# Optimization experiments

Hardware: AMD Instinct MI355X
Metric: run time of the kernel (lower is better)

## Reference

```python
import jax, jax.numpy as jnp
import numpy as np
import math

HEADS = 16
ROPE_BASE = 10000.0


def _alibi_slopes(n):
    # power-of-2 branch of ALiBiBias._get_slopes (n=16 is a power of 2)
    start = 2.0 ** (-(2.0 ** (-(math.log2(n) - 3))))
    return np.array([start * (start ** i) for i in range(n)], dtype=np.float32)


def _rope_cos_sin(T, head_dim):
    # RotaryPositionalEmbedding: inv_freq over even indices, emb = cat(freqs, freqs)
    inv_freq = 1.0 / (ROPE_BASE ** (jnp.arange(0, head_dim, 2, dtype=jnp.float32) / head_dim))
    t = jnp.arange(T, dtype=jnp.float32)
    f = t[:, None] * inv_freq[None, :]            # (T, head_dim//2)
    emb = jnp.concatenate([f, f], axis=-1)        # (T, head_dim)
    # apply_rotary_pos_emb takes cos/sin of emb then strides [0::2]
    cos = jnp.cos(emb)[:, 0::2]                   # (T, head_dim//2)
    sin = jnp.sin(emb)[:, 0::2]
    return cos, sin


def _apply_rope(x, cos, sin):
    # x: (B,H,T,hd); cos/sin: (T, hd//2)
    x1 = x[..., 0::2]
    x2 = x[..., 1::2]
    r1 = x1 * cos - x2 * sin
    r2 = x2 * cos + x1 * sin
    # interleave back: out[...,0::2]=r1, out[...,1::2]=r2
    return jnp.stack([r1, r2], axis=-1).reshape(x.shape)


def setup_inputs() -> dict:
    key = jax.random.key(0)
    k1, k2, k3, k4 = jax.random.split(key, 4)
    B, T, C = 2, 2048, 1024
    x = jax.random.normal(k1, (B, T, C), dtype=jnp.float32)
    W_qkv = jax.random.normal(k2, (C, 3 * C), dtype=jnp.float32) * 0.02
    W_out = jax.random.normal(k3, (C, C), dtype=jnp.float32) * 0.02
    b_out = jax.random.normal(k4, (C,), dtype=jnp.float32) * 0.02
    return {"x": x, "W_qkv": W_qkv, "W_out": W_out, "b_out": b_out}


def reference(x, W_qkv, W_out, b_out):
    B, T, C = x.shape
    H = HEADS
    hd = C // H

    qkv = (x @ W_qkv).reshape(B, T, 3, H, hd)
    qkv = jnp.transpose(qkv, (2, 0, 3, 1, 4))     # (3, B, H, T, hd)
    q, k, v = qkv[0], qkv[1], qkv[2]

    cos, sin = _rope_cos_sin(T, hd)
    q = _apply_rope(q, cos, sin)
    k = _apply_rope(k, cos, sin)

    scores = jnp.einsum('bhqd,bhkd->bhqk', q, k) / jnp.sqrt(jnp.float32(hd))

    # ALiBi bias: -slope_h * |i - j|
    slopes = jnp.asarray(_alibi_slopes(H))        # (H,)
    pos = jnp.arange(T, dtype=jnp.float32)
    dist = jnp.abs(pos[None, :] - pos[:, None])   # (T, T)
    scores = scores - slopes[None, :, None, None] * dist[None, None, :, :]

    attn = jax.nn.softmax(scores, axis=-1)
    out = jnp.einsum('bhqk,bhkd->bhqd', attn, v)  # (B,H,T,hd)
    out = jnp.transpose(out, (0, 2, 1, 3)).reshape(B, T, C)
    out = out @ W_out + b_out
    return out, attn
```

## Files before the change

### kernel.cpp

```cpp
#include <hip/hip_runtime.h>
#include <hip/hip_bf16.h>

typedef __bf16 bf16_t;
typedef __bf16 bf16x8 __attribute__((ext_vector_type(8)));
typedef __bf16 bf16x4 __attribute__((ext_vector_type(4)));
typedef float floatx4 __attribute__((ext_vector_type(4)));

#define NB 2
#define NT 2048
#define NC 1024
#define NH 16
#define HD 64
#define BT (NB*NT)

#define GLL16(g, l) __builtin_amdgcn_global_load_lds( \
    (const __attribute__((address_space(1))) void*)(g), \
    (__attribute__((address_space(3))) void*)(l), 16, 0, 0)

__global__ void k_cvt_x(const float* __restrict__ x, bf16_t* __restrict__ xb, int n){
  int i = (blockIdx.x*blockDim.x + threadIdx.x)*4;
  if (i >= n) return;
  float4 v = *(const float4*)(x+i);
  bf16_t o[4] = {(bf16_t)v.x,(bf16_t)v.y,(bf16_t)v.z,(bf16_t)v.w};
  *(uint2*)(xb+i) = *(const uint2*)o;
}

__global__ void k_cvt_t(const float* __restrict__ in, bf16_t* __restrict__ out, int K, int N){
  __shared__ float tile[32][33];
  int tid = threadIdx.x;
  int kt = blockIdx.y*32, nt = blockIdx.x*32;
  int row = tid>>3, c4 = (tid&7)*4;
  float4 v = *(const float4*)(in + (size_t)(kt+row)*N + nt + c4);
  tile[row][c4+0]=v.x; tile[row][c4+1]=v.y; tile[row][c4+2]=v.z; tile[row][c4+3]=v.w;
  __syncthreads();
  bf16_t o[4];
  #pragma unroll
  for (int i=0;i<4;i++) o[i] = (bf16_t)tile[c4+i][row];
  *(uint2*)(out + (size_t)(nt+row)*K + kt + c4) = *(const uint2*)o;
}

__global__ void k_trv(const bf16_t* __restrict__ qkv, bf16_t* __restrict__ Vt){
  __shared__ float tile[32][33];
  int tid = threadIdx.x;
  int bh = blockIdx.z; int b = bh>>4, h = bh&15;
  int t0 = blockIdx.y*32, d0 = blockIdx.x*32;
  int row = tid>>3, c4 = (tid&7)*4;
  bf16x4 v = *(const bf16x4*)(qkv + (size_t)(b*NT + t0 + row)*3072 + 2048 + h*HD + d0 + c4);
  #pragma unroll
  for (int i=0;i<4;i++) tile[row][c4+i] = (float)v[i];
  __syncthreads();
  bf16x4 o;
  #pragma unroll
  for (int i=0;i<4;i++) o[i] = (bf16_t)tile[c4+i][row];
  *(bf16x4*)(Vt + ((size_t)bh*HD + d0 + row)*NT + t0 + c4) = o;
}

template<bool BIAS, bool OUTBF>
__global__ __launch_bounds__(256) void k_gemm(
    const bf16_t* __restrict__ A, const bf16_t* __restrict__ Bt,
    void* __restrict__ Cv, const float* __restrict__ bias, int M, int N, int K){
  __shared__ __align__(16) bf16_t As[128][64];
  __shared__ __align__(16) bf16_t Bs[128][64];
  int tid = threadIdx.x;
  int wave = tid>>6, lane = tid&63, quad = lane>>4, l15 = lane&15;
  int m0 = blockIdx.y*128, n0 = blockIdx.x*128;
  int wm = (wave>>1)*64, wn = (wave&1)*64;
  floatx4 acc[4][4];
  #pragma unroll
  for(int i=0;i<4;i++)
    #pragma unroll
    for(int j=0;j<4;j++) acc[i][j] = (floatx4){0.f,0.f,0.f,0.f};
  int srow = lane>>3;
  int sslot = (lane&7) ^ srow;
  const bf16_t* Ag = A  + (size_t)(m0 + wave*32 + srow)*K + sslot*8;
  const bf16_t* Bg = Bt + (size_t)(n0 + wave*32 + srow)*K + sslot*8;
  int rs = l15 & 7;
  for (int k0=0; k0<K; k0+=64){
    #pragma unroll
    for (int i=0;i<4;i++){
      GLL16(Ag + (size_t)(i*8)*K + k0, &As[wave*32 + i*8][0]);
      GLL16(Bg + (size_t)(i*8)*K + k0, &Bs[wave*32 + i*8][0]);
    }
    __syncthreads();
    bf16x8 af[2][4], bfr[2][4];
    #pragma unroll
    for (int kk=0;kk<2;kk++){
      #pragma unroll
      for (int mi=0;mi<4;mi++) af[kk][mi]  = *(const bf16x8*)&As[wm+mi*16+l15][8*((kk*4+quad) ^ rs)];
      #pragma unroll
      for (int ni=0;ni<4;ni++) bfr[kk][ni] = *(const bf16x8*)&Bs[wn+ni*16+l15][8*((kk*4+quad) ^ rs)];
    }
    #pragma unroll
    for (int kk=0;kk<2;kk++)
      #pragma unroll
      for (int mi=0;mi<4;mi++)
        #pragma unroll
        for (int ni=0;ni<4;ni++)
          acc[mi][ni] = __builtin_amdgcn_mfma_f32_16x16x32_bf16(af[kk][mi], bfr[kk][ni], acc[mi][ni],0,0,0);
    __syncthreads();
  }
  #pragma unroll
  for (int ni=0;ni<4;ni++){
    int col = n0 + wn + ni*16 + l15;
    float bv = 0.f; if (BIAS) bv = bias[col];
    #pragma unroll
    for (int mi=0;mi<4;mi++){
      int rowb = m0 + wm + mi*16 + quad*4;
      #pragma unroll
      for (int r=0;r<4;r++){
        float v = acc[mi][ni][r] + bv;
        if (OUTBF) ((bf16_t*)Cv)[(size_t)(rowb+r)*N + col] = (bf16_t)v;
        else       ((float*)Cv)[(size_t)(rowb+r)*N + col]  = v;
      }
    }
  }
}

__global__ void k_rope(const bf16_t* __restrict__ qkv, bf16_t* __restrict__ Qb,
                       bf16_t* __restrict__ Kb){
  int p = blockIdx.x*blockDim.x + threadIdx.x;
  int r = p >> 10;
  int c = (p & 1023)*2;
  int s = c >> 10, rem = c & 1023;
  int h = rem >> 6, d = rem & 63, j = d >> 1;
  int b = r >> 11, t = r & 2047;
  float x1 = (float)qkv[(size_t)r*3072 + c];
  float x2 = (float)qkv[(size_t)r*3072 + c + 1];
  float freq = exp2f(-0.8304820237218406f * (float)(j & 15));
  float ang = (float)t * freq;
  float sn, cs;
  sincosf(ang, &sn, &cs);
  float o1 = x1*cs - x2*sn;
  float o2 = x2*cs + x1*sn;
  bf16_t* dst = (s==0) ? Qb : Kb;
  bf16_t o[2] = {(bf16_t)o1, (bf16_t)o2};
  *(unsigned int*)(dst + (size_t)((b*NH + h)*NT + t)*HD + d) = *(const unsigned int*)o;
}

__global__ __launch_bounds__(256) void k_attn(
    const bf16_t* __restrict__ Qb, const bf16_t* __restrict__ Kb, const bf16_t* __restrict__ Vtg,
    float* __restrict__ attn, bf16_t* __restrict__ Ob){
  __shared__ __align__(16) bf16_t Ks[64][64];
  __shared__ __align__(16) bf16_t Vs[64][64];
  __shared__ __align__(16) bf16_t Ps[4][16][64];
  int tid = threadIdx.x;
  int wave = tid>>6, lane = tid&63, quad = lane>>4, l15 = lane&15;
  int qt = blockIdx.x, bh = blockIdx.y;
  int h = bh & (NH-1);
  const float LOG2E = 1.4426950408889634f;
  float slope2 = exp2f(-0.5f*(float)(h+1)) * LOG2E;
  const float c1 = 0.125f * LOG2E;
  int qbase = qt*64 + wave*16;
  const bf16_t* qrow = Qb + ((size_t)bh*NT + qbase + l15)*HD;
  bf16x8 qa0 = *(const bf16x8*)(qrow + quad*8);
  bf16x8 qa1 = *(const bf16x8*)(qrow + 32 + quad*8);
  int srow = lane>>3, sslot = (lane&7) ^ srow;
  const bf16_t* kg = Kb  + ((size_t)bh*NT + wave*16 + srow)*HD + sslot*8;
  const bf16_t* vg = Vtg + ((size_t)bh*HD + wave*16 + srow)*NT + sslot*8;
  const floatx4 z4 = {0.f,0.f,0.f,0.f};
  int rs = l15 & 7;

  float lsum[4] = {0.f,0.f,0.f,0.f};
  for (int k0=0;k0<NT;k0+=64){
    #pragma unroll
    for (int i=0;i<2;i++)
      GLL16(kg + (size_t)(i*8)*HD + (size_t)k0*HD, &Ks[wave*16 + i*8][0]);
    __syncthreads();
    #pragma unroll
    for (int nt=0;nt<4;nt++){
      bf16x8 kb0 = *(const bf16x8*)&Ks[nt*16+l15][8*((quad)   ^ rs)];
      bf16x8 kb1 = *(const bf16x8*)&Ks[nt*16+l15][8*((4+quad) ^ rs)];
      floatx4 sv = __builtin_amdgcn_mfma_f32_16x16x32_bf16(qa0, kb0, z4,0,0,0);
      sv = __builtin_amdgcn_mfma_f32_16x16x32_bf16(qa1, kb1, sv,0,0,0);
      float fk = (float)(qbase + quad*4 - (k0 + nt*16 + l15));
      #pragma unroll
      for (int r=0;r<4;r++){
        float arg = fmaf(sv[r], c1, -slope2*fabsf(fk + (float)r));
        lsum[r] += exp2f(arg);
      }
    }
    __syncthreads();
  }
  #pragma unroll
  for (int r=0;r<4;r++){
    #pragma unroll
    for (int off=1;off<16;off<<=1) lsum[r] += __shfl_xor(lsum[r], off, 16);
  }
  float invl[4];
  #pragma unroll
  for (int r=0;r<4;r++) invl[r] = 1.f / lsum[r];

  floatx4 oacc[4] = {z4,z4,z4,z4};
  float* attnrow = attn + (size_t)bh*NT*NT;
  for (int k0=0;k0<NT;k0+=64){
    #pragma unroll
    for (int i=0;i<2;i++){
      GLL16(kg + (size_t)(i*8)*HD + (size_t)k0*HD, &Ks[wave*16 + i*8][0]);
      GLL16(vg + (size_t)(i*8)*NT + k0,            &Vs[wave*16 + i*8][0]);
    }
    __syncthreads();
    #pragma unroll
    for (int nt=0;nt<4;nt++){
      bf16x8 kb0 = *(const bf16x8*)&Ks[nt*16+l15][8*((quad)   ^ rs)];
      bf16x8 kb1 = *(const bf16x8*)&Ks[nt*16+l15][8*((4+quad) ^ rs)];
      floatx4 sv = __builtin_amdgcn_mfma_f32_16x16x32_bf16(qa0, kb0, z4,0,0,0);
      sv = __builtin_amdgcn_mfma_f32_16x16x32_bf16(qa1, kb1, sv,0,0,0);
      int kpos = k0 + nt*16 + l15;
      float fk = (float)(qbase + quad*4 - kpos);
      #pragma unroll
      for (int r=0;r<4;r++){
        float arg = fmaf(sv[r], c1, -slope2*fabsf(fk + (float)r));
        float pv = exp2f(arg) * invl[r];
        int qpos = qbase + quad*4 + r;
        __builtin_nontemporal_store(pv, &attnrow[(size_t)qpos*NT + kpos]);
        Ps[wave][quad*4+r][ 8*(((nt*2) + (l15>>3)) ^ ((quad*4+r)&7)) + (l15&7) ] = (bf16_t)pv;
      }
    }
    #pragma unroll
    for (int ks=0;ks<2;ks++){
      bf16x8 pa = *(const bf16x8*)&Ps[wave][l15][8*((ks*4+quad) ^ rs)];
      #pragma unroll
      for (int dt=0;dt<4;dt++){
        bf16x8 vb = *(const bf16x8*)&Vs[dt*16+l15][8*((ks*4+quad) ^ rs)];
        oacc[dt] = __builtin_amdgcn_mfma_f32_16x16x32_bf16(pa, vb, oacc[dt],0,0,0);
      }
    }
    __syncthreads();
  }
  int b = bh >> 4;
  #pragma unroll
  for (int dt=0;dt<4;dt++){
    #pragma unroll
    for (int r=0;r<4;r++){
      int t = qbase + quad*4 + r;
      Ob[(size_t)(b*NT + t)*NC + h*HD + dt*16 + l15] = (bf16_t)oacc[dt][r];
    }
  }
}

extern "C" void kernel_launch(void* const* d_in, const int* in_sizes, int n_in,
                              void* d_out, int out_size, void* d_ws, size_t ws_size,
                              hipStream_t stream){
  const float* x    = (const float*)d_in[0];
  const float* Wqkv = (const float*)d_in[1];
  const float* Wout = (const float*)d_in[2];
  const float* bout = (const float*)d_in[3];
  (void)in_sizes; (void)n_in; (void)out_size; (void)ws_size;

  char* ws = (char*)d_ws;
  size_t off = 0;
  auto alloc = [&](size_t elems)->bf16_t* {
    bf16_t* p = (bf16_t*)(ws + off);
    off += ((elems*sizeof(bf16_t) + 255)/256)*256;
    return p;
  };
  bf16_t* Xb   = alloc((size_t)BT*NC);
  bf16_t* Wqt  = alloc((size_t)3*NC*NC);
  bf16_t* Wot  = alloc((size_t)NC*NC);
  bf16_t* QKVb = alloc((size_t)BT*3*NC);
  bf16_t* Qb   = alloc((size_t)NB*NH*NT*HD);
  bf16_t* Kb   = alloc((size_t)NB*NH*NT*HD);
  bf16_t* Vtg  = alloc((size_t)NB*NH*HD*NT);
  bf16_t* Ob   = alloc((size_t)BT*NC);

  k_cvt_x<<<(BT*NC/4)/256, 256, 0, stream>>>(x, Xb, BT*NC);
  k_cvt_t<<<dim3(3*NC/32, NC/32), 256, 0, stream>>>(Wqkv, Wqt, NC, 3*NC);
  k_cvt_t<<<dim3(NC/32,   NC/32), 256, 0, stream>>>(Wout, Wot, NC, NC);
  k_gemm<false,true><<<dim3(3*NC/128, BT/128), 256, 0, stream>>>(Xb, Wqt, (void*)QKVb, nullptr, BT, 3*NC, NC);
  k_rope<<<(BT*1024)/256, 256, 0, stream>>>(QKVb, Qb, Kb);
  k_trv<<<dim3(HD/32, NT/32, NB*NH), 256, 0, stream>>>(QKVb, Vtg);
  float* attn = (float*)d_out + (size_t)BT*NC;
  k_attn<<<dim3(NT/64, NB*NH), 256, 0, stream>>>(Qb, Kb, Vtg, attn, Ob);
  k_gemm<true,false><<<dim3(NC/128, BT/128), 256, 0, stream>>>(Ob, Wot, d_out, bout, BT, NC, NC);
}
```

Baseline: 750.1 us.

## Double attention query tile per block, shrink out-proj GEMM M-tile, use fast sincos

The attention kernel now runs 8 waves per block over 128 query rows, so each K/V tile staged in LDS serves twice as many queries and global K/V traffic is halved. The GEMM is templated on the M-tile so the output projection uses 64-row tiles, doubling its block count for better CU occupancy. RoPE switches to the fast __sincosf intrinsic, which costs some accuracy at large angles. Attention now launches fewer, larger blocks, and the kernel is likely dominated by the fp32 attn matrix writes.

```diff
diff --git a/kernel.cpp b/kernel.cpp
--- a/kernel.cpp
+++ b/kernel.cpp
@@ -55,45 +55,47 @@
   *(bf16x4*)(Vt + ((size_t)bh*HD + d0 + row)*NT + t0 + c4) = o;
 }
 
-template<bool BIAS, bool OUTBF>
+template<int MI, bool BIAS, bool OUTBF>
 __global__ __launch_bounds__(256) void k_gemm(
     const bf16_t* __restrict__ A, const bf16_t* __restrict__ Bt,
     void* __restrict__ Cv, const float* __restrict__ bias, int M, int N, int K){
-  __shared__ __align__(16) bf16_t As[128][64];
+  constexpr int BM = MI*32;
+  __shared__ __align__(16) bf16_t As[BM][64];
   __shared__ __align__(16) bf16_t Bs[128][64];
   int tid = threadIdx.x;
   int wave = tid>>6, lane = tid&63, quad = lane>>4, l15 = lane&15;
-  int m0 = blockIdx.y*128, n0 = blockIdx.x*128;
-  int wm = (wave>>1)*64, wn = (wave&1)*64;
-  floatx4 acc[4][4];
-  #pragma unroll
-  for(int i=0;i<4;i++)
+  int m0 = blockIdx.y*BM, n0 = blockIdx.x*128;
+  int wm = (wave>>1)*(MI*16), wn = (wave&1)*64;
+  floatx4 acc[MI][4];
+  #pragma unroll
+  for(int i=0;i<MI;i++)
     #pragma unroll
     for(int j=0;j<4;j++) acc[i][j] = (floatx4){0.f,0.f,0.f,0.f};
   int srow = lane>>3;
   int sslot = (lane&7) ^ srow;
-  const bf16_t* Ag = A  + (size_t)(m0 + wave*32 + srow)*K + sslot*8;
+  const bf16_t* Ag = A  + (size_t)(m0 + wave*(MI*8) + srow)*K + sslot*8;
   const bf16_t* Bg = Bt + (size_t)(n0 + wave*32 + srow)*K + sslot*8;
   int rs = l15 & 7;
   for (int k0=0; k0<K; k0+=64){
     #pragma unroll
-    for (int i=0;i<4;i++){
-      GLL16(Ag + (size_t)(i*8)*K + k0, &As[wave*32 + i*8][0]);
+    for (int i=0;i<MI;i++)
+      GLL16(Ag + (size_t)(i*8)*K + k0, &As[wave*(MI*8) + i*8][0]);
+    #pragma unroll
+    for (int i=0;i<4;i++)
       GLL16(Bg + (size_t)(i*8)*K + k0, &Bs[wave*32 + i*8][0]);
-    }
-    __syncthreads();
-    bf16x8 af[2][4], bfr[2][4];
+    __syncthreads();
+    bf16x8 af[2][MI], bfr[2][4];
     #pragma unroll
     for (int kk=0;kk<2;kk++){
       #pragma unroll
-      for (int mi=0;mi<4;mi++) af[kk][mi]  = *(const bf16x8*)&As[wm+mi*16+l15][8*((kk*4+quad) ^ rs)];
-      #pragma unroll
-      for (int ni=0;ni<4;ni++) bfr[kk][ni] = *(const bf16x8*)&Bs[wn+ni*16+l15][8*((kk*4+quad) ^ rs)];
+      for (int mi=0;mi<MI;mi++) af[kk][mi]  = *(const bf16x8*)&As[wm+mi*16+l15][8*((kk*4+quad) ^ rs)];
+      #pragma unroll
+      for (int ni=0;ni<4;ni++)  bfr[kk][ni] = *(const bf16x8*)&Bs[wn+ni*16+l15][8*((kk*4+quad) ^ rs)];
     }
     #pragma unroll
     for (int kk=0;kk<2;kk++)
       #pragma unroll
-      for (int mi=0;mi<4;mi++)
+      for (int mi=0;mi<MI;mi++)
         #pragma unroll
         for (int ni=0;ni<4;ni++)
           acc[mi][ni] = __builtin_amdgcn_mfma_f32_16x16x32_bf16(af[kk][mi], bfr[kk][ni], acc[mi][ni],0,0,0);
@@ -104,7 +106,7 @@
     int col = n0 + wn + ni*16 + l15;
     float bv = 0.f; if (BIAS) bv = bias[col];
     #pragma unroll
-    for (int mi=0;mi<4;mi++){
+    for (int mi=0;mi<MI;mi++){
       int rowb = m0 + wm + mi*16 + quad*4;
       #pragma unroll
       for (int r=0;r<4;r++){
@@ -129,7 +131,7 @@
   float freq = exp2f(-0.8304820237218406f * (float)(j & 15));
   float ang = (float)t * freq;
   float sn, cs;
-  sincosf(ang, &sn, &cs);
+  __sincosf(ang, &sn, &cs);
   float o1 = x1*cs - x2*sn;
   float o2 = x2*cs + x1*sn;
   bf16_t* dst = (s==0) ? Qb : Kb;
@@ -137,12 +139,12 @@
   *(unsigned int*)(dst + (size_t)((b*NH + h)*NT + t)*HD + d) = *(const unsigned int*)o;
 }
 
-__global__ __launch_bounds__(256) void k_attn(
+__global__ __launch_bounds__(512) void k_attn(
     const bf16_t* __restrict__ Qb, const bf16_t* __restrict__ Kb, const bf16_t* __restrict__ Vtg,
     float* __restrict__ attn, bf16_t* __restrict__ Ob){
   __shared__ __align__(16) bf16_t Ks[64][64];
   __shared__ __align__(16) bf16_t Vs[64][64];
-  __shared__ __align__(16) bf16_t Ps[4][16][64];
+  __shared__ __align__(16) bf16_t Ps[8][16][64];
   int tid = threadIdx.x;
   int wave = tid>>6, lane = tid&63, quad = lane>>4, l15 = lane&15;
   int qt = blockIdx.x, bh = blockIdx.y;
@@ -150,21 +152,19 @@
   const float LOG2E = 1.4426950408889634f;
   float slope2 = exp2f(-0.5f*(float)(h+1)) * LOG2E;
   const float c1 = 0.125f * LOG2E;
-  int qbase = qt*64 + wave*16;
+  int qbase = qt*128 + wave*16;
   const bf16_t* qrow = Qb + ((size_t)bh*NT + qbase + l15)*HD;
   bf16x8 qa0 = *(const bf16x8*)(qrow + quad*8);
   bf16x8 qa1 = *(const bf16x8*)(qrow + 32 + quad*8);
   int srow = lane>>3, sslot = (lane&7) ^ srow;
-  const bf16_t* kg = Kb  + ((size_t)bh*NT + wave*16 + srow)*HD + sslot*8;
-  const bf16_t* vg = Vtg + ((size_t)bh*HD + wave*16 + srow)*NT + sslot*8;
+  const bf16_t* kg = Kb  + ((size_t)bh*NT + wave*8 + srow)*HD + sslot*8;
+  const bf16_t* vg = Vtg + ((size_t)bh*HD + wave*8 + srow)*NT + sslot*8;
   const floatx4 z4 = {0.f,0.f,0.f,0.f};
   int rs = l15 & 7;
 
   float lsum[4] = {0.f,0.f,0.f,0.f};
   for (int k0=0;k0<NT;k0+=64){
-    #pragma unroll
-    for (int i=0;i<2;i++)
-      GLL16(kg + (size_t)(i*8)*HD + (size_t)k0*HD, &Ks[wave*16 + i*8][0]);
+    GLL16(kg + (size_t)k0*HD, &Ks[wave*8][0]);
     __syncthreads();
     #pragma unroll
     for (int nt=0;nt<4;nt++){
@@ -193,11 +193,8 @@
   floatx4 oacc[4] = {z4,z4,z4,z4};
   float* attnrow = attn + (size_t)bh*NT*NT;
   for (int k0=0;k0<NT;k0+=64){
-    #pragma unroll
-    for (int i=0;i<2;i++){
-      GLL16(kg + (size_t)(i*8)*HD + (size_t)k0*HD, &Ks[wave*16 + i*8][0]);
-      GLL16(vg + (size_t)(i*8)*NT + k0,            &Vs[wave*16 + i*8][0]);
-    }
+    GLL16(kg + (size_t)k0*HD, &Ks[wave*8][0]);
+    GLL16(vg + k0,            &Vs[wave*8][0]);
     __syncthreads();
     #pragma unroll
     for (int nt=0;nt<4;nt++){
@@ -266,10 +263,10 @@
   k_cvt_x<<<(BT*NC/4)/256, 256, 0, stream>>>(x, Xb, BT*NC);
   k_cvt_t<<<dim3(3*NC/32, NC/32), 256, 0, stream>>>(Wqkv, Wqt, NC, 3*NC);
   k_cvt_t<<<dim3(NC/32,   NC/32), 256, 0, stream>>>(Wout, Wot, NC, NC);
-  k_gemm<false,true><<<dim3(3*NC/128, BT/128), 256, 0, stream>>>(Xb, Wqt, (void*)QKVb, nullptr, BT, 3*NC, NC);
+  k_gemm<4,false,true><<<dim3(3*NC/128, BT/128), 256, 0, stream>>>(Xb, Wqt, (void*)QKVb, nullptr, BT, 3*NC, NC);
   k_rope<<<(BT*1024)/256, 256, 0, stream>>>(QKVb, Qb, Kb);
   k_trv<<<dim3(HD/32, NT/32, NB*NH), 256, 0, stream>>>(QKVb, Vtg);
   float* attn = (float*)d_out + (size_t)BT*NC;
-  k_attn<<<dim3(NT/64, NB*NH), 256, 0, stream>>>(Qb, Kb, Vtg, attn, Ob);
-  k_gemm<true,false><<<dim3(NC/128, BT/128), 256, 0, stream>>>(Ob, Wot, d_out, bout, BT, NC, NC);
-}
+  k_attn<<<dim3(NT/128, NB*NH), 512, 0, stream>>>(Qb, Kb, Vtg, attn, Ob);
+  k_gemm<2,true,false><<<dim3(NC/128, BT/64), 256, 0, stream>>>(Ob, Wot, d_out, bout, BT, NC, NC);
+}
```

Measured after the change: 758.7 us. No clear change (+1.2%).
